# Performance work log

Measured on AMD Instinct MI355X. Metric: run time of the kernel, lower is better.

## Reference

```python
import jax, jax.numpy as jnp
import numpy as np

N_WIRES = 4
DIM = 1 << N_WIRES  # 16
N_PATCH = 14 * 14   # 196


def _random_unitary_16(seed=0):
    # Deterministic surrogate for tq.RandomLayer(n_ops=8): a fixed random
    # real orthogonal 16x16 operator applied to the 4-qubit state.
    rng = np.random.default_rng(seed)
    q, _ = np.linalg.qr(rng.standard_normal((DIM, DIM)))
    return jnp.asarray(q, dtype=jnp.float32)


def _linear_params(rng, fan_in, fan_out):
    bound = 1.0 / np.sqrt(fan_in)
    w = rng.uniform(-bound, bound, size=(fan_out, fan_in)).astype(np.float32)
    b = rng.uniform(-bound, bound, size=(fan_out,)).astype(np.float32)
    return jnp.asarray(w), jnp.asarray(b)


def setup_inputs() -> dict:
    key = jax.random.key(0)
    x = jax.random.normal(key, (8192, 784), dtype=jnp.float32)
    rng = np.random.default_rng(1)
    fc1_w, fc1_b = _linear_params(rng, 784, 120)
    fc2_w, fc2_b = _linear_params(rng, 120, 84)
    fc3_w, fc3_b = _linear_params(rng, 84, 1)
    return {
        "x": x,
        "U": _random_unitary_16(),
        "fc1_w": fc1_w, "fc1_b": fc1_b,
        "fc2_w": fc2_w, "fc2_b": fc2_b,
        "fc3_w": fc3_w, "fc3_b": fc3_b,
    }


def _quantum_filter(x, U):
    # x: [b, 784] -> 2x2 patches in row-major order, per-patch wire data
    # [x[r,c], x[r,c+1], x[r+1,c], x[r+1,c+1]]
    b = x.shape[0]
    xp = x.reshape(b, 14, 2, 14, 2).transpose(0, 1, 3, 2, 4).reshape(b, N_PATCH, N_WIRES)
    # Encoder: RY(theta_w) on wire w starting from |0000> -> product state
    c = jnp.cos(0.5 * xp)  # [b, p, 4]
    s = jnp.sin(0.5 * xp)
    a = jnp.stack([c, s], axis=-1)  # [b, p, 4, 2] per-wire amplitudes
    psi = jnp.einsum("bpi,bpj,bpk,bpl->bpijkl",
                     a[:, :, 0], a[:, :, 1], a[:, :, 2], a[:, :, 3])
    psi = psi.reshape(b, N_PATCH, DIM)  # wire 0 = most significant bit
    # Fixed random layer (16x16 unitary)
    psi = jnp.einsum("ij,bpj->bpi", U, psi)
    # PauliZ expectation per wire: sum_i |psi_i|^2 * (1 - 2*bit_w(i))
    idx = jnp.arange(DIM)
    bits = (idx[:, None] >> (N_WIRES - 1 - jnp.arange(N_WIRES))) & 1  # [16, 4]
    zsign = (1 - 2 * bits).astype(psi.dtype)
    meas = jnp.einsum("bpi,iw->bpw", psi * psi, zsign)  # [b, p, 4]
    return meas.reshape(b, N_PATCH * N_WIRES)  # [b, 784]


def reference(x, U, fc1_w, fc1_b, fc2_w, fc2_b, fc3_w, fc3_b):
    feats = _quantum_filter(x, U)
    h = jax.nn.relu(feats @ fc1_w.T + fc1_b)
    h = jax.nn.relu(h @ fc2_w.T + fc2_b)
    logits = (h @ fc3_w.T + fc3_b)[:, 0]  # [b], matches inputs.squeeze()
    # = P(|1>) = (1 + sin(theta)) / 2 (analytic, shot-noise-free)
    exp_val = 0.5 * (1.0 + jnp.sin(logits))
    p = jax.nn.sigmoid(exp_val)
    return jnp.concatenate([p, 1.0 - p], axis=-1)  # [2*b], matches torch.cat on 1-D
```

## Files before the change

kernel.cpp:

```cpp
#include <hip/hip_runtime.h>
#include <hip/hip_bf16.h>
#include <math.h>


#define BATCH   8192
#define NPATCH  196
#define KPAD    800
#define H1LD    132
#define NCHUNKS ((BATCH * NPATCH) / 64)

typedef __attribute__((ext_vector_type(8))) short bfrag;
typedef __attribute__((ext_vector_type(4))) short bfrag4;
typedef __attribute__((ext_vector_type(4))) float f32x4;

#if __has_builtin(__builtin_amdgcn_mfma_f32_16x16x16bf16_1k)
#define USE_X16 1
#else
#define USE_X16 0
#endif

static __device__ __forceinline__ unsigned short f2bf(float f) {
    __hip_bfloat16 h = __float2bfloat16(f);
    return __builtin_bit_cast(unsigned short, h);
}
static __device__ __forceinline__ unsigned int pkbf(float lo, float hi) {
    return ((unsigned int)f2bf(hi) << 16) | (unsigned int)f2bf(lo);
}

__global__ __launch_bounds__(256) void w1prep_kernel(
    const float* __restrict__ w1, unsigned short* __restrict__ w1B)
{
    int t = blockIdx.x * 256 + threadIdx.x;
    if (t >= 128 * KPAD) return;
    int n = t / KPAD;
    int k = t - n * KPAD;
    float v = (n < 120 && k < 784) ? w1[n * 784 + k] : 0.f;
    w1B[t] = f2bf(v);
}

__global__ __launch_bounds__(256) void qfilter_kernel(
    const float* __restrict__ x, const float* __restrict__ U,
    unsigned short* __restrict__ featsB)
{
    __shared__ __align__(16) unsigned short psiL[4][64][16];

    const int lane = threadIdx.x & 63;
    const int wv   = threadIdx.x >> 6;
    const int lrow = lane & 15;
    const int lgrp = lane >> 4;
    const int base = (blockIdx.x * 4 + wv) * 64;

#if USE_X16
    bfrag4 Uf16;
    {
        union { bfrag4 f; unsigned int u[2]; } uu;
        float4 a = *reinterpret_cast<const float4*>(U + lrow * 16 + lgrp * 4);
        uu.u[0] = pkbf(a.x, a.y);
        uu.u[1] = pkbf(a.z, a.w);
        Uf16 = uu.f;
    }
    bfrag4 Zf;
    {
        union { bfrag4 f; unsigned int u[2]; } zz;
        if (lrow < 4) {
            float z[4];
#pragma unroll
            for (int j = 0; j < 4; ++j) {
                int k = 4 * lgrp + j;
                z[j] = ((k >> (3 - lrow)) & 1) ? -1.f : 1.f;
            }
            zz.u[0] = pkbf(z[0], z[1]);
            zz.u[1] = pkbf(z[2], z[3]);
        } else {
            zz.u[0] = zz.u[1] = 0u;
        }
        Zf = zz.f;
    }
#else
    bfrag Uf;
    {
        union { bfrag f; unsigned int u[4]; } uu;
        if (lgrp < 2) {
            float4 a = *reinterpret_cast<const float4*>(U + lrow * 16 + lgrp * 8);
            float4 b = *reinterpret_cast<const float4*>(U + lrow * 16 + lgrp * 8 + 4);
            uu.u[0] = pkbf(a.x, a.y); uu.u[1] = pkbf(a.z, a.w);
            uu.u[2] = pkbf(b.x, b.y); uu.u[3] = pkbf(b.z, b.w);
        } else {
            uu.u[0] = uu.u[1] = uu.u[2] = uu.u[3] = 0u;
        }
        Uf = uu.f;
    }
#endif

    {
        int item = base + lane;
        int b  = item / NPATCH;
        int p  = item - b * NPATCH;
        int pr = p / 14;
        int pc = p - pr * 14;
        const float* xr = x + (size_t)b * 784 + pr * 56 + pc * 2;
        float2 xa = *reinterpret_cast<const float2*>(xr);
        float2 xb = *reinterpret_cast<const float2*>(xr + 28);

        float s0, c0, s1, c1, s2, c2, s3, c3;
        __sincosf(0.5f * xa.x, &s0, &c0);
        __sincosf(0.5f * xa.y, &s1, &c1);
        __sincosf(0.5f * xb.x, &s2, &c2);
        __sincosf(0.5f * xb.y, &s3, &c3);

        float t01[4] = {c0 * c1, c0 * s1, s0 * c1, s0 * s1};
        float t23[4] = {c2 * c3, c2 * s3, s2 * c3, s2 * s3};

        unsigned int pw[8];
#pragma unroll
        for (int q = 0; q < 8; ++q) {
            float plo = t01[(2 * q) >> 2]     * t23[(2 * q) & 3];
            float phv = t01[(2 * q + 1) >> 2] * t23[(2 * q + 1) & 3];
            pw[q] = pkbf(plo, phv);
        }
        *reinterpret_cast<uint4*>(&psiL[wv][lane][0]) =
            make_uint4(pw[0], pw[1], pw[2], pw[3]);
        *reinterpret_cast<uint4*>(&psiL[wv][lane][8]) =
            make_uint4(pw[4], pw[5], pw[6], pw[7]);
    }

#pragma unroll
    for (int sub = 0; sub < 4; ++sub) {
        int item16 = base + sub * 16 + lrow;
#if USE_X16
        bfrag4 Pf = *reinterpret_cast<const bfrag4*>(
            &psiL[wv][sub * 16 + lrow][lgrp * 4]);
        f32x4 dz = {0.f, 0.f, 0.f, 0.f};
        f32x4 d = __builtin_amdgcn_mfma_f32_16x16x16bf16_1k(Uf16, Pf, dz, 0, 0, 0);
        union { bfrag4 f; unsigned int u[2]; } qq;
        qq.u[0] = pkbf(d[0] * d[0], d[1] * d[1]);
        qq.u[1] = pkbf(d[2] * d[2], d[3] * d[3]);
        f32x4 m = __builtin_amdgcn_mfma_f32_16x16x16bf16_1k(Zf, qq.f, dz, 0, 0, 0);
        if (lgrp == 0) {
            int b16 = item16 / NPATCH;
            int p16 = item16 - b16 * NPATCH;
            uint2 o2;
            o2.x = pkbf(m[0], m[1]);
            o2.y = pkbf(m[2], m[3]);
            *reinterpret_cast<uint2*>(featsB + (size_t)b16 * KPAD + p16 * 4) = o2;
        }
#else
        bfrag Bf = {};
        if (lgrp < 2)
            Bf = *reinterpret_cast<const bfrag*>(
                &psiL[wv][sub * 16 + lrow][lgrp * 8]);
        f32x4 dz = {0.f, 0.f, 0.f, 0.f};
        f32x4 d = __builtin_amdgcn_mfma_f32_16x16x32_bf16(Uf, Bf, dz, 0, 0, 0);
        float q0 = d[0] * d[0], q1 = d[1] * d[1];
        float q2 = d[2] * d[2], q3 = d[3] * d[3];
        float sAll = (q0 + q1) + (q2 + q3);
        float uu2  = (q0 + q1) - (q2 + q3);
        float vv2  = (q0 - q1) + (q2 - q3);
        float t    = __shfl_xor(sAll, 16);
        float Aa   = sAll + t;
        float Bb   = ((threadIdx.x & 16)) ? (t - sAll) : (sAll - t);
        t = __shfl_xor(Aa, 32);
        float mw0 = ((threadIdx.x & 32)) ? (t - Aa) : (Aa - t);
        float mw1 = Bb + __shfl_xor(Bb, 32);
        float u16 = uu2 + __shfl_xor(uu2, 16);
        float mw2 = u16 + __shfl_xor(u16, 32);
        float v16 = vv2 + __shfl_xor(vv2, 16);
        float mw3 = v16 + __shfl_xor(v16, 32);
        if (lgrp == 0) {
            int b16 = item16 / NPATCH;
            int p16 = item16 - b16 * NPATCH;
            ushort4 o;
            o.x = f2bf(mw0); o.y = f2bf(mw1);
            o.z = f2bf(mw2); o.w = f2bf(mw3);
            *reinterpret_cast<ushort4*>(featsB + (size_t)b16 * KPAD + p16 * 4) = o;
        }
#endif
    }
}

__global__ __launch_bounds__(256) void tail_kernel(
    const unsigned short* __restrict__ featsB,
    const unsigned short* __restrict__ w1B,
    const float* __restrict__ b1,
    const float* __restrict__ w2, const float* __restrict__ b2,
    const float* __restrict__ w3, const float* __restrict__ b3,
    float* __restrict__ out)
{
    __shared__ __align__(16) float h1L[16 * H1LD];
    __shared__ __align__(16) float h2L[16 * 84];

    const int tid  = threadIdx.x;
    const int lane = tid & 63;
    const int wv   = tid >> 6;
    const int lrow = lane & 15;
    const int lgrp = lane >> 4;
    const int m0   = blockIdx.x * 16;

    {
        const unsigned short* fA =
            featsB + (size_t)(m0 + lrow) * KPAD + lgrp * 8;
        const unsigned short* bp0 =
            w1B + (size_t)(wv * 32 + lrow) * KPAD + lgrp * 8;
        const unsigned short* bp1 = bp0 + 16 * KPAD;

        f32x4 acc0 = {}, acc1 = {};
        for (int k0 = 0; k0 < KPAD; k0 += 32) {
            bfrag a   = *reinterpret_cast<const bfrag*>(fA + k0);
            bfrag b0  = *reinterpret_cast<const bfrag*>(bp0 + k0);
            bfrag b1f = *reinterpret_cast<const bfrag*>(bp1 + k0);
            acc0 = __builtin_amdgcn_mfma_f32_16x16x32_bf16(a, b0, acc0, 0, 0, 0);
            acc1 = __builtin_amdgcn_mfma_f32_16x16x32_bf16(a, b1f, acc1, 0, 0, 0);
        }
        f32x4 accs[2] = {acc0, acc1};
#pragma unroll
        for (int nj = 0; nj < 2; ++nj) {
            int col = wv * 32 + nj * 16 + lrow;
            if (col < 120) {
                float bias = b1[col];
#pragma unroll
                for (int rr = 0; rr < 4; ++rr) {
                    int row = lgrp * 4 + rr;
                    h1L[row * H1LD + col] = fmaxf(accs[nj][rr] + bias, 0.f);
                }
            }
        }
    }
    __syncthreads();

    for (int e = tid; e < 16 * 21; e += 256) {
        int r  = e / 21;
        int nq = e - r * 21;
        int n0 = nq * 4;
        float4 bias = *reinterpret_cast<const float4*>(b2 + n0);
        float accv[4] = {bias.x, bias.y, bias.z, bias.w};
#pragma unroll
        for (int kq = 0; kq < 30; ++kq) {
            float4 a = *reinterpret_cast<const float4*>(&h1L[r * H1LD + kq * 4]);
#pragma unroll
            for (int nn = 0; nn < 4; ++nn) {
                const float4 wvv = *reinterpret_cast<const float4*>(
                    w2 + (size_t)(n0 + nn) * 120 + kq * 4);
                accv[nn] = fmaf(a.x, wvv.x, accv[nn]);
                accv[nn] = fmaf(a.y, wvv.y, accv[nn]);
                accv[nn] = fmaf(a.z, wvv.z, accv[nn]);
                accv[nn] = fmaf(a.w, wvv.w, accv[nn]);
            }
        }
        float4 o;
        o.x = fmaxf(accv[0], 0.f);
        o.y = fmaxf(accv[1], 0.f);
        o.z = fmaxf(accv[2], 0.f);
        o.w = fmaxf(accv[3], 0.f);
        *reinterpret_cast<float4*>(&h2L[r * 84 + n0]) = o;
    }
    __syncthreads();

    if (tid < 16) {
        int r = tid;
        float acc = b3[0];
#pragma unroll
        for (int kq = 0; kq < 21; ++kq) {
            float4 a   = *reinterpret_cast<const float4*>(&h2L[r * 84 + kq * 4]);
            float4 wvv = *reinterpret_cast<const float4*>(w3 + kq * 4);
            acc = fmaf(a.x, wvv.x, acc);
            acc = fmaf(a.y, wvv.y, acc);
            acc = fmaf(a.z, wvv.z, acc);
            acc = fmaf(a.w, wvv.w, acc);
        }
        float ev = 0.5f * (1.0f + __sinf(acc));
        float pp = 1.0f / (1.0f + __expf(-ev));
        out[m0 + r]         = pp;
        out[BATCH + m0 + r] = 1.0f - pp;
    }
}

extern "C" void kernel_launch(void* const* d_in, const int* in_sizes, int n_in,
                              void* d_out, int out_size, void* d_ws, size_t ws_size,
                              hipStream_t stream)
{
    (void)in_sizes; (void)n_in; (void)out_size; (void)ws_size;
    const float* x  = (const float*)d_in[0];
    const float* U  = (const float*)d_in[1];
    const float* w1 = (const float*)d_in[2];
    const float* b1 = (const float*)d_in[3];
    const float* w2 = (const float*)d_in[4];
    const float* b2 = (const float*)d_in[5];
    const float* w3 = (const float*)d_in[6];
    const float* b3 = (const float*)d_in[7];
    float* out = (float*)d_out;

    unsigned short* w1B    = (unsigned short*)d_ws;
    unsigned short* featsB = w1B + (size_t)128 * KPAD;

    w1prep_kernel<<<dim3((128 * KPAD + 255) / 256), dim3(256), 0, stream>>>(w1, w1B);
    qfilter_kernel<<<dim3(NCHUNKS / 4), dim3(256), 0, stream>>>(x, U, featsB);
    tail_kernel<<<dim3(BATCH / 16), dim3(256), 0, stream>>>(
        featsB, w1B, b1, w2, b2, w3, b3, out);
}
```

Measured before the change: 136.5 us.

## Split fc1 GEMM over K slices and add separate reduction head kernel

Splits the fc1 MFMA GEMM into five K slices across a 2D grid, staging feature tiles in LDS and writing fp32 partial sums to workspace. A new head kernel sums the partials, applies bias and ReLU, and runs fc2/fc3 with w2 and w3 staged in shared memory. The aim is more parallelism for the short-K-loop GEMM and removing repeated global w2 reads, at the cost of an extra launch, extra global traffic for partials, and larger workspace use.

```diff
diff --git a/kernel.cpp b/kernel.cpp
--- a/kernel.cpp
+++ b/kernel.cpp
@@ -6,6 +6,8 @@
 #define BATCH   8192
 #define NPATCH  196
 #define KPAD    800
+#define KSLICE  160
+#define FLD3    168
 #define H1LD    132
 #define NCHUNKS ((BATCH * NPATCH) / 64)
 
@@ -178,16 +180,12 @@
     }
 }
 
-__global__ __launch_bounds__(256) void tail_kernel(
+__global__ __launch_bounds__(256) void fc1_kernel(
     const unsigned short* __restrict__ featsB,
     const unsigned short* __restrict__ w1B,
-    const float* __restrict__ b1,
-    const float* __restrict__ w2, const float* __restrict__ b2,
-    const float* __restrict__ w3, const float* __restrict__ b3,
-    float* __restrict__ out)
-{
-    __shared__ __align__(16) float h1L[16 * H1LD];
-    __shared__ __align__(16) float h2L[16 * 84];
+    float* __restrict__ hp)
+{
+    __shared__ __align__(16) unsigned short featsL[16 * FLD3];
 
     const int tid  = threadIdx.x;
     const int lane = tid & 63;
@@ -195,35 +193,85 @@
     const int lrow = lane & 15;
     const int lgrp = lane >> 4;
     const int m0   = blockIdx.x * 16;
-
-    {
-        const unsigned short* fA =
-            featsB + (size_t)(m0 + lrow) * KPAD + lgrp * 8;
-        const unsigned short* bp0 =
-            w1B + (size_t)(wv * 32 + lrow) * KPAD + lgrp * 8;
-        const unsigned short* bp1 = bp0 + 16 * KPAD;
-
-        f32x4 acc0 = {}, acc1 = {};
-        for (int k0 = 0; k0 < KPAD; k0 += 32) {
-            bfrag a   = *reinterpret_cast<const bfrag*>(fA + k0);
-            bfrag b0  = *reinterpret_cast<const bfrag*>(bp0 + k0);
-            bfrag b1f = *reinterpret_cast<const bfrag*>(bp1 + k0);
-            acc0 = __builtin_amdgcn_mfma_f32_16x16x32_bf16(a, b0, acc0, 0, 0, 0);
-            acc1 = __builtin_amdgcn_mfma_f32_16x16x32_bf16(a, b1f, acc1, 0, 0, 0);
-        }
-        f32x4 accs[2] = {acc0, acc1};
-#pragma unroll
-        for (int nj = 0; nj < 2; ++nj) {
-            int col = wv * 32 + nj * 16 + lrow;
-            if (col < 120) {
-                float bias = b1[col];
-#pragma unroll
-                for (int rr = 0; rr < 4; ++rr) {
-                    int row = lgrp * 4 + rr;
-                    h1L[row * H1LD + col] = fmaxf(accs[nj][rr] + bias, 0.f);
-                }
-            }
-        }
+    const int ks   = blockIdx.y;
+    const int kb   = ks * KSLICE;
+
+    for (int t = tid; t < 320; t += 256) {
+        int row = t / 20;
+        int c   = t - row * 20;
+        uint4 v = *reinterpret_cast<const uint4*>(
+            featsB + (size_t)(m0 + row) * KPAD + kb + c * 8);
+        *reinterpret_cast<uint4*>(&featsL[row * FLD3 + c * 8]) = v;
+    }
+    __syncthreads();
+
+    const unsigned short* fA  = &featsL[lrow * FLD3 + lgrp * 8];
+    const unsigned short* bp0 = w1B + (size_t)(wv * 32 + lrow) * KPAD + kb + lgrp * 8;
+    const unsigned short* bp1 = bp0 + 16 * KPAD;
+
+    f32x4 acc0 = {}, acc1 = {};
+#pragma unroll
+    for (int k0 = 0; k0 < KSLICE; k0 += 32) {
+        bfrag a   = *reinterpret_cast<const bfrag*>(fA + k0);
+        bfrag b0  = *reinterpret_cast<const bfrag*>(bp0 + k0);
+        bfrag b1f = *reinterpret_cast<const bfrag*>(bp1 + k0);
+        acc0 = __builtin_amdgcn_mfma_f32_16x16x32_bf16(a, b0, acc0, 0, 0, 0);
+        acc1 = __builtin_amdgcn_mfma_f32_16x16x32_bf16(a, b1f, acc1, 0, 0, 0);
+    }
+
+    float* hps = hp + (size_t)ks * (BATCH * 128);
+    f32x4 accs[2] = {acc0, acc1};
+#pragma unroll
+    for (int nj = 0; nj < 2; ++nj) {
+        int col = wv * 32 + nj * 16 + lrow;
+        if (col < 120) {
+#pragma unroll
+            for (int rr = 0; rr < 4; ++rr)
+                hps[(size_t)(m0 + lgrp * 4 + rr) * 128 + col] = accs[nj][rr];
+        }
+    }
+}
+
+__global__ __launch_bounds__(256) void head_kernel(
+    const float* __restrict__ hp,
+    const float* __restrict__ b1,
+    const float* __restrict__ w2, const float* __restrict__ b2,
+    const float* __restrict__ w3, const float* __restrict__ b3,
+    float* __restrict__ out)
+{
+    __shared__ __align__(16) float h1L[16 * H1LD];
+    __shared__ __align__(16) float w2L[84 * 120];
+    __shared__ __align__(16) float h2L[16 * 84];
+    __shared__ __align__(16) float w3L[88];
+
+    const int tid = threadIdx.x;
+    const int m0  = blockIdx.x * 16;
+
+    for (int t = tid; t < 2520; t += 256) {
+        *reinterpret_cast<float4*>(&w2L[t * 4]) =
+            *reinterpret_cast<const float4*>(w2 + t * 4);
+    }
+    if (tid < 21) {
+        *reinterpret_cast<float4*>(&w3L[tid * 4]) =
+            *reinterpret_cast<const float4*>(w3 + tid * 4);
+    }
+
+    for (int t = tid; t < 480; t += 256) {
+        int r  = t / 30;
+        int nq = t - r * 30;
+        const float* p0 = hp + (size_t)(m0 + r) * 128 + nq * 4;
+        float4 s  = *reinterpret_cast<const float4*>(p0);
+        float4 s1 = *reinterpret_cast<const float4*>(p0 + 1 * BATCH * 128);
+        float4 s2 = *reinterpret_cast<const float4*>(p0 + 2 * BATCH * 128);
+        float4 s3 = *reinterpret_cast<const float4*>(p0 + 3 * BATCH * 128);
+        float4 s4 = *reinterpret_cast<const float4*>(p0 + 4 * BATCH * 128);
+        float4 bias = *reinterpret_cast<const float4*>(b1 + nq * 4);
+        float4 o;
+        o.x = fmaxf(s.x + s1.x + s2.x + s3.x + s4.x + bias.x, 0.f);
+        o.y = fmaxf(s.y + s1.y + s2.y + s3.y + s4.y + bias.y, 0.f);
+        o.z = fmaxf(s.z + s1.z + s2.z + s3.z + s4.z + bias.z, 0.f);
+        o.w = fmaxf(s.w + s1.w + s2.w + s3.w + s4.w + bias.w, 0.f);
+        *reinterpret_cast<float4*>(&h1L[r * H1LD + nq * 4]) = o;
     }
     __syncthreads();
 
@@ -239,7 +287,7 @@
 #pragma unroll
             for (int nn = 0; nn < 4; ++nn) {
                 const float4 wvv = *reinterpret_cast<const float4*>(
-                    w2 + (size_t)(n0 + nn) * 120 + kq * 4);
+                    &w2L[(n0 + nn) * 120 + kq * 4]);
                 accv[nn] = fmaf(a.x, wvv.x, accv[nn]);
                 accv[nn] = fmaf(a.y, wvv.y, accv[nn]);
                 accv[nn] = fmaf(a.z, wvv.z, accv[nn]);
@@ -261,7 +309,7 @@
 #pragma unroll
         for (int kq = 0; kq < 21; ++kq) {
             float4 a   = *reinterpret_cast<const float4*>(&h2L[r * 84 + kq * 4]);
-            float4 wvv = *reinterpret_cast<const float4*>(w3 + kq * 4);
+            float4 wvv = *reinterpret_cast<const float4*>(&w3L[kq * 4]);
             acc = fmaf(a.x, wvv.x, acc);
             acc = fmaf(a.y, wvv.y, acc);
             acc = fmaf(a.z, wvv.z, acc);
@@ -291,9 +339,11 @@
 
     unsigned short* w1B    = (unsigned short*)d_ws;
     unsigned short* featsB = w1B + (size_t)128 * KPAD;
+    float*          hp     = (float*)(featsB + (size_t)BATCH * KPAD);
 
     w1prep_kernel<<<dim3((128 * KPAD + 255) / 256), dim3(256), 0, stream>>>(w1, w1B);
     qfilter_kernel<<<dim3(NCHUNKS / 4), dim3(256), 0, stream>>>(x, U, featsB);
-    tail_kernel<<<dim3(BATCH / 16), dim3(256), 0, stream>>>(
-        featsB, w1B, b1, w2, b2, w3, b3, out);
-}
+    fc1_kernel<<<dim3(BATCH / 16, 5), dim3(256), 0, stream>>>(featsB, w1B, hp);
+    head_kernel<<<dim3(BATCH / 16), dim3(256), 0, stream>>>(
+        hp, b1, w2, b2, w3, b3, out);
+}
```

Result: faster. 125.9 us (-7.8%).
